# Performance work log

Measured on AMD Instinct MI355X. Metric: run time of the kernel, lower is better.

Reference implementation:

```python
import jax, jax.numpy as jnp
import numpy as np

BS, S, F, H = 512, 128, 136, 128
DISCOUNT = 0.99


def _gru_cell(x, h, Wih, Whh, bih, bhh):
    # torch.nn.GRUCell math; gate order r, z, n
    gi = x @ Wih.T + bih
    gh = h @ Whh.T + bhh
    i_r, i_z, i_n = jnp.split(gi, 3, axis=-1)
    h_r, h_z, h_n = jnp.split(gh, 3, axis=-1)
    r = jax.nn.sigmoid(i_r + h_r)
    z = jax.nn.sigmoid(i_z + h_z)
    n = jnp.tanh(i_n + r * h_n)
    return (1.0 - z) * n + z * h


def _run(batch_ranks, label, fnn_W1, fnn_b1, fnn_W2, fnn_b2,
         cnt_W1, cnt_b1, cnt_W2, cnt_b2, com_W1, com_b1, com_W2, com_b2,
         gru_Wih, gru_Whh, gru_bih, gru_bhh):
    bs, S_, F_ = batch_ranks.shape
    dt = batch_ranks.dtype
    # fnn (Dropout is identity in eval): Linear-ReLU-Linear-Sigmoid
    doc = jax.nn.sigmoid(jax.nn.relu(batch_ranks @ fnn_W1 + fnn_b1) @ fnn_W2 + fnn_b2)  # [bs,S,H]
    H_ = doc.shape[-1]
    pointer = jnp.arange(S_)[None, :]
    h0 = jnp.zeros((bs, H_), dt)
    mask0 = jnp.ones((bs, S_), bool)

    def step(carry, i):
        h, mask = carry
        m3 = mask[:, :, None]
        # stats over still-unselected docs (masked_select equivalent)
        mx = jnp.max(jnp.where(m3, batch_ranks, -jnp.inf), axis=1)            # [bs,F]
        cnt = jnp.sum(mask, axis=1, keepdims=True).astype(dt)
        mn = jnp.sum(jnp.where(m3, batch_ranks, 0.0), axis=1) / cnt           # [bs,F]
        cr = jax.nn.sigmoid(jax.nn.relu(jnp.concatenate([mx, mn], axis=1) @ cnt_W1 + cnt_b1) @ cnt_W2 + cnt_b2)  # [bs,H]
        state = jnp.concatenate([doc,
                                 jnp.broadcast_to(cr[:, None, :], doc.shape),
                                 jnp.broadcast_to(h[:, None, :], doc.shape)], axis=2)  # [bs,S,3H]
        scores = (jax.nn.relu(state @ com_W1 + com_b1) @ com_W2 + com_b2)[..., 0]      # [bs,S]
        p = jax.nn.softmax(scores, axis=-1)        # softmax BEFORE masking, as in source
        p = jnp.where(mask, p, -jnp.inf)
        idx = jnp.argmax(p, axis=-1)               # [bs]
        prob = jnp.max(p, axis=-1)                 # [bs]
        sel = pointer == idx[:, None]              # [bs,S] bool one-hot
        sel_label = jnp.sum(jnp.where(sel, label, 0.0), axis=1)
        reward = (2.0 ** sel_label - 1.0) / jnp.log2(i.astype(dt) + 2.0)
        sel_doc = jnp.einsum('bs,bsh->bh', sel.astype(dt), doc)
        h_new = _gru_cell(sel_doc, h, gru_Wih, gru_Whh, gru_bih, gru_bhh)
        return (h_new, mask & (~sel)), (prob, idx, reward)

    (_, _), (probs, indices, rewards) = jax.lax.scan(step, (h0, mask0), jnp.arange(S_))
    probs = probs.T          # [bs,S]
    indices = indices.T      # [bs,S]
    rewards = rewards.T      # [bs,S]
    rewards = rewards * (DISCOUNT ** jnp.arange(S_, dtype=dt))[None, :]
    R = jnp.flip(jnp.cumsum(jnp.flip(rewards, 1), axis=1), 1)
    loss = -jnp.sum(R * jnp.log(probs))
    sp_loss = -jnp.sum(jax.nn.softmax(label, axis=1) * jax.nn.log_softmax(probs, axis=1))
    ranking = 0.9 ** jnp.argsort(indices, axis=-1).astype(dt)
    return ranking, loss, sp_loss


def setup_inputs() -> dict:
    key = jax.random.key(0)
    ks = jax.random.split(key, 12)
    def lin(k, fi, fo):
        return (jax.random.normal(k, (fi, fo), jnp.float32) / np.sqrt(fi)).astype(jnp.float32)
    return {
        'batch_ranks': jax.random.normal(ks[0], (BS, S, F), jnp.float32),
        'label': jax.random.uniform(ks[1], (BS, S), jnp.float32, 0.0, 4.0),
        'fnn_W1': lin(ks[2], F, H), 'fnn_b1': jnp.zeros((H,), jnp.float32),
        'fnn_W2': lin(ks[3], H, H), 'fnn_b2': jnp.zeros((H,), jnp.float32),
        'cnt_W1': lin(ks[4], 2 * F, H), 'cnt_b1': jnp.zeros((H,), jnp.float32),
        'cnt_W2': lin(ks[5], H, H), 'cnt_b2': jnp.zeros((H,), jnp.float32),
        'com_W1': lin(ks[6], 3 * H, H), 'com_b1': jnp.zeros((H,), jnp.float32),
        'com_W2': lin(ks[7], H, 1), 'com_b2': jnp.zeros((1,), jnp.float32),
        'gru_Wih': (jax.random.normal(ks[8], (3 * H, H), jnp.float32) / np.sqrt(H)),
        'gru_Whh': (jax.random.normal(ks[9], (3 * H, H), jnp.float32) / np.sqrt(H)),
        'gru_bih': jnp.zeros((3 * H,), jnp.float32),
        'gru_bhh': jnp.zeros((3 * H,), jnp.float32),
    }


def reference(batch_ranks, label, fnn_W1, fnn_b1, fnn_W2, fnn_b2,
              cnt_W1, cnt_b1, cnt_W2, cnt_b2, com_W1, com_b1, com_W2, com_b2,
              gru_Wih, gru_Whh, gru_bih, gru_bhh):
    ranking, loss, sp_loss = _run(batch_ranks, label, fnn_W1, fnn_b1, fnn_W2, fnn_b2,
                                  cnt_W1, cnt_b1, cnt_W2, cnt_b2, com_W1, com_b1,
                                  com_W2, com_b2, gru_Wih, gru_Whh, gru_bih, gru_bhh)
    return ranking
```

## Files before the change

kernel.cpp:

```cpp
#include <hip/hip_runtime.h>
#include <math.h>

#define BSZ 512
#define SEQ 128
#define FF  136
#define HH  128

__global__ __launch_bounds__(256) void k_transpose384(const float* __restrict__ A,
                                                      float* __restrict__ At) {
    int i = blockIdx.x * 256 + threadIdx.x;
    if (i < 384 * 128) {
        int r = i >> 7, c = i & 127;
        At[c * 384 + r] = A[i];
    }
}

__global__ __launch_bounds__(256) void k_docvgi(
    const float* __restrict__ br,
    const float* __restrict__ fW1, const float* __restrict__ fb1,
    const float* __restrict__ fW2, const float* __restrict__ fb2,
    const float* __restrict__ comW1,
    const float* __restrict__ WihT, const float* __restrict__ bih,
    float* __restrict__ V, float* __restrict__ GI)
{
    __shared__ float xs[32][FF];
    __shared__ float hs[32][HH];
    __shared__ float ds[32][HH];
    int row0 = blockIdx.x * 32;
    int t = threadIdx.x;
    const float* src = br + (size_t)row0 * FF;
    for (int i = t; i < 32 * FF; i += 256) xs[i / FF][i % FF] = src[i];
    __syncthreads();
    int j = t & 127, rg = t >> 7;
    float acc[16];
#pragma unroll
    for (int r = 0; r < 16; r++) acc[r] = 0.f;
    for (int k = 0; k < FF; k++) {
        float w = fW1[k * HH + j];
#pragma unroll
        for (int r = 0; r < 16; r++) acc[r] += xs[rg + 2 * r][k] * w;
    }
    {
        float bb = fb1[j];
#pragma unroll
        for (int r = 0; r < 16; r++) hs[rg + 2 * r][j] = fmaxf(acc[r] + bb, 0.f);
    }
    __syncthreads();
#pragma unroll
    for (int r = 0; r < 16; r++) acc[r] = 0.f;
    for (int k = 0; k < HH; k++) {
        float w = fW2[k * HH + j];
#pragma unroll
        for (int r = 0; r < 16; r++) acc[r] += hs[rg + 2 * r][k] * w;
    }
    {
        float bb = fb2[j];
#pragma unroll
        for (int r = 0; r < 16; r++)
            ds[rg + 2 * r][j] = 1.f / (1.f + expf(-(acc[r] + bb)));
    }
    __syncthreads();
#pragma unroll
    for (int r = 0; r < 16; r++) acc[r] = 0.f;
    for (int k = 0; k < HH; k++) {
        float w = comW1[k * HH + j];
#pragma unroll
        for (int r = 0; r < 16; r++) acc[r] += ds[rg + 2 * r][k] * w;
    }
#pragma unroll
    for (int r = 0; r < 16; r++) V[(size_t)(row0 + rg + 2 * r) * HH + j] = acc[r];
    for (int p = 0; p < 3; p++) {
        int jj = p * HH + j;
#pragma unroll
        for (int r = 0; r < 16; r++) acc[r] = 0.f;
        for (int k = 0; k < HH; k++) {
            float w = WihT[k * 384 + jj];
#pragma unroll
            for (int r = 0; r < 16; r++) acc[r] += ds[rg + 2 * r][k] * w;
        }
        float bb = bih[jj];
#pragma unroll
        for (int r = 0; r < 16; r++)
            GI[(size_t)(row0 + rg + 2 * r) * 384 + jj] = acc[r] + bb;
    }
}

__global__ __launch_bounds__(256) void k_scan(
    const float* __restrict__ br,
    const float* __restrict__ cntW1, const float* __restrict__ cntb1,
    const float* __restrict__ cntW2, const float* __restrict__ cntb2,
    const float* __restrict__ comW1, const float* __restrict__ comb1,
    const float* __restrict__ comW2,
    const float* __restrict__ WhhT, const float* __restrict__ gbhh,
    const float* __restrict__ V, const float* __restrict__ GI,
    float* __restrict__ out)
{
    __shared__ float  Vl[SEQ][HH + 1];
    __shared__ float  hS[HH], crS[HH], a1S[HH], uS[HH], scS[SEQ], c2S[HH];
    __shared__ float  mxS[FF], mnS[FF];
    __shared__ double smS[FF];
    __shared__ int    mxiS[FF];
    __shared__ int    maskS[SEQ];
    __shared__ float  pp[2][3][HH];
    __shared__ int    selS;

    int b = blockIdx.x;
    int t = threadIdx.x;
    const float* brB = br + (size_t)b * SEQ * FF;
    const float* Vb  = V  + (size_t)b * SEQ * HH;
    const float* GIb = GI + (size_t)b * SEQ * 3 * HH;

    for (int i = t; i < SEQ * HH; i += 256) { int s = i >> 7, j = i & 127; Vl[s][j] = Vb[i]; }
    if (t < HH)  { hS[t] = 0.f; c2S[t] = comW2[t]; }
    if (t < SEQ) maskS[t] = 1;
    if (t < FF) {
        double sm = 0.0; float mx = -__builtin_huge_valf(); int mi = 0;
        for (int s = 0; s < SEQ; s++) {
            float v = brB[s * FF + t];
            sm += (double)v;
            if (v > mx) { mx = v; mi = s; }
        }
        smS[t] = sm; mxS[t] = mx; mxiS[t] = mi;
    }
    __syncthreads();

    int j = t & 127, hf = t >> 7;

    for (int i = 0; i < SEQ; i++) {
        float cntf = (float)(SEQ - i);
        if (t < FF) mnS[t] = ((float)smS[t]) / cntf;
        __syncthreads();

        {
            float acc = 0.f;
            if (hf == 0) {
                for (int k = 0; k < FF; k++) acc += mxS[k] * cntW1[k * HH + j];
            } else {
                for (int k = 0; k < FF; k++) acc += mnS[k] * cntW1[(FF + k) * HH + j];
            }
            pp[hf][0][j] = acc;
        }
        __syncthreads();
        if (t < HH) { float v = pp[0][0][t] + pp[1][0][t] + cntb1[t]; a1S[t] = fmaxf(v, 0.f); }
        __syncthreads();

        {
            float acc = 0.f;
            for (int k = hf * 64; k < hf * 64 + 64; k++) acc += a1S[k] * cntW2[k * HH + j];
            pp[hf][0][j] = acc;
        }
        __syncthreads();
        if (t < HH) { float v = pp[0][0][t] + pp[1][0][t] + cntb2[t]; crS[t] = 1.f / (1.f + expf(-v)); }
        __syncthreads();

        {
            const float* srcv = (hf == 0) ? crS : hS;
            const float* W = comW1 + (size_t)(HH + hf * HH) * HH;
            float acc = 0.f;
            for (int k = 0; k < HH; k++) acc += srcv[k] * W[k * HH + j];
            pp[hf][0][j] = acc;
        }
        __syncthreads();
        if (t < HH) uS[t] = pp[0][0][t] + pp[1][0][t] + comb1[t];
        __syncthreads();

        {
            float acc = 0.f;
            for (int k = hf * 64; k < hf * 64 + 64; k++)
                acc += c2S[k] * fmaxf(Vl[j][k] + uS[k], 0.f);
            pp[hf][0][j] = acc;
        }
        __syncthreads();
        if (t < SEQ) scS[t] = pp[0][0][t] + pp[1][0][t];
        __syncthreads();

        if (t < 64) {
            float v1 = maskS[t]      ? scS[t]      : -__builtin_huge_valf();
            float v2 = maskS[t + 64] ? scS[t + 64] : -__builtin_huge_valf();
            float v; int idx;
            if (v2 > v1) { v = v2; idx = t + 64; } else { v = v1; idx = t; }
            for (int off = 32; off >= 1; off >>= 1) {
                float ov = __shfl_down(v, off);
                int   oi = __shfl_down(idx, off);
                if (ov > v || (ov == v && oi < idx)) { v = ov; idx = oi; }
            }
            if (t == 0) {
                selS = idx;
                maskS[idx] = 0;
                out[(size_t)b * SEQ + idx] = powf(0.9f, (float)i);
            }
        }
        __syncthreads();
        int sel = selS;

        if (t < FF) {
            float rv = brB[sel * FF + t];
            smS[t] -= (double)rv;
            if (sel == mxiS[t] && i < SEQ - 1) {
                float mx = -__builtin_huge_valf(); int mi = 0;
                for (int s = 0; s < SEQ; s++) {
                    if (maskS[s]) { float v = brB[s * FF + t]; if (v > mx) { mx = v; mi = s; } }
                }
                mxS[t] = mx; mxiS[t] = mi;
            }
        }

        {
            float ar = 0.f, az = 0.f, an = 0.f;
            for (int k = hf * 64; k < hf * 64 + 64; k++) {
                float hv = hS[k];
                const float* Wr = WhhT + (size_t)k * 384;
                ar += hv * Wr[j];
                az += hv * Wr[HH + j];
                an += hv * Wr[2 * HH + j];
            }
            pp[hf][0][j] = ar; pp[hf][1][j] = az; pp[hf][2][j] = an;
        }
        __syncthreads();
        if (t < HH) {
            const float* gir = GIb + (size_t)sel * 384;
            float ghr = pp[0][0][t] + pp[1][0][t] + gbhh[t];
            float ghz = pp[0][1][t] + pp[1][1][t] + gbhh[HH + t];
            float ghn = pp[0][2][t] + pp[1][2][t] + gbhh[2 * HH + t];
            float r = 1.f / (1.f + expf(-(gir[t] + ghr)));
            float z = 1.f / (1.f + expf(-(gir[HH + t] + ghz)));
            float n = tanhf(gir[2 * HH + t] + r * ghn);
            float hn = (1.f - z) * n + z * hS[t];
            scS[t] = hn;
        }
        __syncthreads();
        if (t < HH) hS[t] = scS[t];
        __syncthreads();
    }
}

extern "C" void kernel_launch(void* const* d_in, const int* in_sizes, int n_in,
                              void* d_out, int out_size, void* d_ws, size_t ws_size,
                              hipStream_t stream) {
    (void)in_sizes; (void)n_in; (void)out_size; (void)ws_size;
    const float* br    = (const float*)d_in[0];
    const float* fnnW1 = (const float*)d_in[2];
    const float* fnnb1 = (const float*)d_in[3];
    const float* fnnW2 = (const float*)d_in[4];
    const float* fnnb2 = (const float*)d_in[5];
    const float* cntW1 = (const float*)d_in[6];
    const float* cntb1 = (const float*)d_in[7];
    const float* cntW2 = (const float*)d_in[8];
    const float* cntb2 = (const float*)d_in[9];
    const float* comW1 = (const float*)d_in[10];
    const float* comb1 = (const float*)d_in[11];
    const float* comW2 = (const float*)d_in[12];
    const float* Wih   = (const float*)d_in[14];
    const float* Whh   = (const float*)d_in[15];
    const float* bih   = (const float*)d_in[16];
    const float* bhh   = (const float*)d_in[17];

    float* ws   = (float*)d_ws;
    float* V    = ws;
    float* GI   = ws + 8388608;
    float* WihT = ws + 8388608 + 25165824;
    float* WhhT = WihT + 49152;

    hipLaunchKernelGGL(k_transpose384, dim3(192), dim3(256), 0, stream, Wih, WihT);
    hipLaunchKernelGGL(k_transpose384, dim3(192), dim3(256), 0, stream, Whh, WhhT);
    hipLaunchKernelGGL(k_docvgi, dim3(2048), dim3(256), 0, stream,
                       br, fnnW1, fnnb1, fnnW2, fnnb2, comW1, WihT, bih, V, GI);
    hipLaunchKernelGGL(k_scan, dim3(BSZ), dim3(256), 0, stream,
                       br, cntW1, cntb1, cntW2, cntb2, comW1, comb1, comW2,
                       WhhT, bhh, V, GI, (float*)d_out);
}
```

Measured before the change: 3.470 ms.

## Process two batches per block and update cnt first layer incrementally

The scan kernel now handles two batch rows per 1024-thread block, so each weight load serves both rows and more threads share each matvec. The first cnt layer is kept as running double-precision pre-activations for the max and sum parts. Each step subtracts the selected document's contribution and adds corrections only for features whose max changed, instead of recomputing the full 272x128 matvec. This adds more LDS use (two V tiles), atomics for the change list, and many barriers per step, and it may lower occupancy.

```diff
diff --git a/kernel.cpp b/kernel.cpp
--- a/kernel.cpp
+++ b/kernel.cpp
@@ -85,7 +85,7 @@
     }
 }
 
-__global__ __launch_bounds__(256) void k_scan(
+__global__ __launch_bounds__(1024, 4) void k_scan2(
     const float* __restrict__ br,
     const float* __restrict__ cntW1, const float* __restrict__ cntb1,
     const float* __restrict__ cntW2, const float* __restrict__ cntb2,
@@ -95,141 +95,217 @@
     const float* __restrict__ V, const float* __restrict__ GI,
     float* __restrict__ out)
 {
-    __shared__ float  Vl[SEQ][HH + 1];
-    __shared__ float  hS[HH], crS[HH], a1S[HH], uS[HH], scS[SEQ], c2S[HH];
-    __shared__ float  mxS[FF], mnS[FF];
-    __shared__ double smS[FF];
-    __shared__ int    mxiS[FF];
-    __shared__ int    maskS[SEQ];
-    __shared__ float  pp[2][3][HH];
-    __shared__ int    selS;
-
-    int b = blockIdx.x;
-    int t = threadIdx.x;
-    const float* brB = br + (size_t)b * SEQ * FF;
-    const float* Vb  = V  + (size_t)b * SEQ * HH;
-    const float* GIb = GI + (size_t)b * SEQ * 3 * HH;
-
-    for (int i = t; i < SEQ * HH; i += 256) { int s = i >> 7, j = i & 127; Vl[s][j] = Vb[i]; }
-    if (t < HH)  { hS[t] = 0.f; c2S[t] = comW2[t]; }
-    if (t < SEQ) maskS[t] = 1;
-    if (t < FF) {
-        double sm = 0.0; float mx = -__builtin_huge_valf(); int mi = 0;
-        for (int s = 0; s < SEQ; s++) {
-            float v = brB[s * FF + t];
-            sm += (double)v;
-            if (v > mx) { mx = v; mi = s; }
-        }
-        smS[t] = sm; mxS[t] = mx; mxiS[t] = mi;
-    }
-    __syncthreads();
-
-    int j = t & 127, hf = t >> 7;
+    __shared__ double svS[2][HH];
+    __shared__ double mxvS[2][HH];
+    __shared__ float  Vl[2][SEQ][HH + 1];
+    __shared__ float  pp[2][8][HH];
+    __shared__ float  ghp[2][2][384];
+    __shared__ float  hS[2][HH], crS[2][HH], uS[2][HH];
+    __shared__ float  scS[2][SEQ];
+    __shared__ float  mxS[2][FF];
+    __shared__ int    mxiS[2][FF];
+    __shared__ int    maskS[2][SEQ];
+    __shared__ int    chgF[2][FF];
+    __shared__ float  chgD[2][FF];
+    __shared__ int    chgN[2];
+    __shared__ float  pw[SEQ], c2S[HH];
+    __shared__ int    selS[2];
+
+    const int b0 = blockIdx.x * 2;
+    const int t  = threadIdx.x;
+    const float* brB0 = br + (size_t)b0 * SEQ * FF;
+    const float* brB1 = br + (size_t)(b0 + 1) * SEQ * FF;
+
+    for (int g = 0; g < 2; g++) {
+        const float* Vb = V + (size_t)(b0 + g) * SEQ * HH;
+        for (int idx = t; idx < SEQ * HH; idx += 1024)
+            Vl[g][idx >> 7][idx & 127] = Vb[idx];
+    }
+    {
+        int g = t >> 9, r = t & 511;
+        if (r < FF) {
+            const float* bp = (g ? brB1 : brB0) + r;
+            float cs = 0.f; float mx = -__builtin_huge_valf(); int mi = 0;
+            for (int s = 0; s < SEQ; s++) {
+                float v = bp[s * FF];
+                cs += v;
+                if (v > mx) { mx = v; mi = s; }
+            }
+            mxS[g][r] = mx; mxiS[g][r] = mi; chgD[g][r] = cs;
+        }
+    }
+    if (t < SEQ) pw[t] = powf(0.9f, (float)t);
+    if (t < HH)  c2S[t] = comW2[t];
+    if (t < 256) { int g = t >> 7, j = t & 127; hS[g][j] = 0.f; maskS[g][j] = 1; }
+    __syncthreads();
+    if (t < 256) {
+        int g = t >> 7, j = t & 127;
+        double am = 0.0, as = 0.0;
+        for (int f = 0; f < FF; f++) {
+            am += (double)mxS[g][f]  * (double)cntW1[f * HH + j];
+            as += (double)chgD[g][f] * (double)cntW1[(FF + f) * HH + j];
+        }
+        mxvS[g][j] = am; svS[g][j] = as;
+    }
+    __syncthreads();
 
     for (int i = 0; i < SEQ; i++) {
-        float cntf = (float)(SEQ - i);
-        if (t < FF) mnS[t] = ((float)smS[t]) / cntf;
+        if (t < 256) {
+            int g = t >> 7, j = t & 127;
+            if (j == 0) chgN[g] = 0;
+            float pre = (float)(mxvS[g][j] + svS[g][j] / (double)(SEQ - i)) + cntb1[j];
+            scS[g][j] = fmaxf(pre, 0.f);
+        }
         __syncthreads();
 
         {
+            int kg = t >> 7, j = t & 127, k0 = kg * 16;
+            float a0 = 0.f, a1 = 0.f;
+            for (int m = 0; m < 16; m++) {
+                int k = k0 + m;
+                float w = cntW2[k * HH + j];
+                a0 += scS[0][k] * w; a1 += scS[1][k] * w;
+            }
+            pp[0][kg][j] = a0; pp[1][kg][j] = a1;
+        }
+        __syncthreads();
+        if (t < 256) {
+            int g = t >> 7, j = t & 127;
+            float s = pp[g][0][j] + pp[g][1][j] + pp[g][2][j] + pp[g][3][j]
+                    + pp[g][4][j] + pp[g][5][j] + pp[g][6][j] + pp[g][7][j] + cntb2[j];
+            crS[g][j] = 1.f / (1.f + expf(-s));
+        }
+        __syncthreads();
+
+        {
+            int kg = t >> 7, j = t & 127, k0 = kg * 32;
+            const float* base = comW1 + (size_t)(HH + k0) * HH + j;
+            const float* s0p, * s1p;
+            if (kg < 4) { s0p = crS[0] + k0; s1p = crS[1] + k0; }
+            else        { s0p = hS[0] + (k0 - 128); s1p = hS[1] + (k0 - 128); }
+            float a0 = 0.f, a1 = 0.f;
+            for (int m = 0; m < 32; m++) {
+                float w = base[m * HH];
+                a0 += s0p[m] * w; a1 += s1p[m] * w;
+            }
+            pp[0][kg][j] = a0; pp[1][kg][j] = a1;
+        }
+        __syncthreads();
+        if (t < 256) {
+            int g = t >> 7, j = t & 127;
+            uS[g][j] = pp[g][0][j] + pp[g][1][j] + pp[g][2][j] + pp[g][3][j]
+                     + pp[g][4][j] + pp[g][5][j] + pp[g][6][j] + pp[g][7][j] + comb1[j];
+        }
+        __syncthreads();
+
+        {
+            int g = t >> 9, r = t & 511, kg = r >> 7, s = r & 127, k0 = kg * 32;
             float acc = 0.f;
-            if (hf == 0) {
-                for (int k = 0; k < FF; k++) acc += mxS[k] * cntW1[k * HH + j];
-            } else {
-                for (int k = 0; k < FF; k++) acc += mnS[k] * cntW1[(FF + k) * HH + j];
-            }
-            pp[hf][0][j] = acc;
-        }
-        __syncthreads();
-        if (t < HH) { float v = pp[0][0][t] + pp[1][0][t] + cntb1[t]; a1S[t] = fmaxf(v, 0.f); }
+            for (int m = 0; m < 32; m++) {
+                int k = k0 + m;
+                acc += c2S[k] * fmaxf(Vl[g][s][k] + uS[g][k], 0.f);
+            }
+            pp[g][kg][s] = acc;
+        }
+        __syncthreads();
+        if (t < 256) {
+            int g = t >> 7, s = t & 127;
+            scS[g][s] = pp[g][0][s] + pp[g][1][s] + pp[g][2][s] + pp[g][3][s];
+        }
         __syncthreads();
 
         {
-            float acc = 0.f;
-            for (int k = hf * 64; k < hf * 64 + 64; k++) acc += a1S[k] * cntW2[k * HH + j];
-            pp[hf][0][j] = acc;
-        }
-        __syncthreads();
-        if (t < HH) { float v = pp[0][0][t] + pp[1][0][t] + cntb2[t]; crS[t] = 1.f / (1.f + expf(-v)); }
-        __syncthreads();
-
-        {
-            const float* srcv = (hf == 0) ? crS : hS;
-            const float* W = comW1 + (size_t)(HH + hf * HH) * HH;
-            float acc = 0.f;
-            for (int k = 0; k < HH; k++) acc += srcv[k] * W[k * HH + j];
-            pp[hf][0][j] = acc;
-        }
-        __syncthreads();
-        if (t < HH) uS[t] = pp[0][0][t] + pp[1][0][t] + comb1[t];
-        __syncthreads();
-
-        {
-            float acc = 0.f;
-            for (int k = hf * 64; k < hf * 64 + 64; k++)
-                acc += c2S[k] * fmaxf(Vl[j][k] + uS[k], 0.f);
-            pp[hf][0][j] = acc;
-        }
-        __syncthreads();
-        if (t < SEQ) scS[t] = pp[0][0][t] + pp[1][0][t];
-        __syncthreads();
-
-        if (t < 64) {
-            float v1 = maskS[t]      ? scS[t]      : -__builtin_huge_valf();
-            float v2 = maskS[t + 64] ? scS[t + 64] : -__builtin_huge_valf();
-            float v; int idx;
-            if (v2 > v1) { v = v2; idx = t + 64; } else { v = v1; idx = t; }
-            for (int off = 32; off >= 1; off >>= 1) {
-                float ov = __shfl_down(v, off);
-                int   oi = __shfl_down(idx, off);
-                if (ov > v || (ov == v && oi < idx)) { v = ov; idx = oi; }
-            }
-            if (t == 0) {
-                selS = idx;
-                maskS[idx] = 0;
-                out[(size_t)b * SEQ + idx] = powf(0.9f, (float)i);
-            }
-        }
-        __syncthreads();
-        int sel = selS;
-
-        if (t < FF) {
-            float rv = brB[sel * FF + t];
-            smS[t] -= (double)rv;
-            if (sel == mxiS[t] && i < SEQ - 1) {
-                float mx = -__builtin_huge_valf(); int mi = 0;
-                for (int s = 0; s < SEQ; s++) {
-                    if (maskS[s]) { float v = brB[s * FF + t]; if (v > mx) { mx = v; mi = s; } }
-                }
-                mxS[t] = mx; mxiS[t] = mi;
-            }
-        }
-
-        {
-            float ar = 0.f, az = 0.f, an = 0.f;
-            for (int k = hf * 64; k < hf * 64 + 64; k++) {
-                float hv = hS[k];
-                const float* Wr = WhhT + (size_t)k * 384;
-                ar += hv * Wr[j];
-                az += hv * Wr[HH + j];
-                an += hv * Wr[2 * HH + j];
-            }
-            pp[hf][0][j] = ar; pp[hf][1][j] = az; pp[hf][2][j] = an;
-        }
-        __syncthreads();
-        if (t < HH) {
-            const float* gir = GIb + (size_t)sel * 384;
-            float ghr = pp[0][0][t] + pp[1][0][t] + gbhh[t];
-            float ghz = pp[0][1][t] + pp[1][1][t] + gbhh[HH + t];
-            float ghn = pp[0][2][t] + pp[1][2][t] + gbhh[2 * HH + t];
-            float r = 1.f / (1.f + expf(-(gir[t] + ghr)));
-            float z = 1.f / (1.f + expf(-(gir[HH + t] + ghz)));
-            float n = tanhf(gir[2 * HH + t] + r * ghn);
-            float hn = (1.f - z) * n + z * hS[t];
-            scS[t] = hn;
-        }
-        __syncthreads();
-        if (t < HH) hS[t] = scS[t];
+            int gg = -1, lane = 0;
+            if (t < 64)                { gg = 0; lane = t; }
+            else if (t >= 512 && t < 576) { gg = 1; lane = t - 512; }
+            if (gg >= 0) {
+                float v1 = maskS[gg][lane]      ? scS[gg][lane]      : -__builtin_huge_valf();
+                float v2 = maskS[gg][lane + 64] ? scS[gg][lane + 64] : -__builtin_huge_valf();
+                float v; int idx;
+                if (v2 > v1) { v = v2; idx = lane + 64; } else { v = v1; idx = lane; }
+                for (int off = 32; off >= 1; off >>= 1) {
+                    float ov = __shfl_down(v, off);
+                    int   oi = __shfl_down(idx, off);
+                    if (ov > v || (ov == v && oi < idx)) { v = ov; idx = oi; }
+                }
+                if (lane == 0) {
+                    selS[gg] = idx;
+                    maskS[gg][idx] = 0;
+                    out[(size_t)(b0 + gg) * SEQ + idx] = pw[i];
+                }
+            }
+        }
+        __syncthreads();
+
+        if (i < SEQ - 1) {
+            int g = t >> 9, r = t & 511;
+            int sel = selS[g];
+            const float* brB = g ? brB1 : brB0;
+            if (r < FF) {
+                int f = r;
+                if (sel == mxiS[g][f]) {
+                    float om = mxS[g][f];
+                    float mx = -__builtin_huge_valf(); int mi = 0;
+                    for (int s = 0; s < SEQ; s++) {
+                        if (maskS[g][s]) {
+                            float v = brB[s * FF + f];
+                            if (v > mx) { mx = v; mi = s; }
+                        }
+                    }
+                    mxS[g][f] = mx; mxiS[g][f] = mi;
+                    int e = atomicAdd(&chgN[g], 1);
+                    chgF[g][e] = f; chgD[g][e] = mx - om;
+                }
+            } else if (r >= 256) {
+                int kg = (r >> 7) - 2, j = r & 127;
+                const float* brow = brB + (size_t)sel * FF;
+                float acc = 0.f;
+                int k0 = kg * 68;
+                for (int m = 0; m < 68; m++) {
+                    int k = k0 + m;
+                    acc += brow[k] * cntW1[(FF + k) * HH + j];
+                }
+                pp[g][4 + kg][j] = acc;
+            }
+        }
+        __syncthreads();
+
+        if (i < SEQ - 1 && t < 256) {
+            int g = t >> 7, j = t & 127;
+            svS[g][j] -= (double)(pp[g][4][j] + pp[g][5][j]);
+            int n = chgN[g];
+            double acc = mxvS[g][j];
+            for (int e = 0; e < n; e++)
+                acc += (double)chgD[g][e] * (double)cntW1[chgF[g][e] * HH + j];
+            mxvS[g][j] = acc;
+        }
+        __syncthreads();
+
+        if (i < SEQ - 1) {
+            if (t < 768) {
+                int kg = t / 384, jj = t % 384, k0 = kg * 64;
+                const float* Wp = WhhT + (size_t)k0 * 384 + jj;
+                float a0 = 0.f, a1 = 0.f;
+                for (int m = 0; m < 64; m++) {
+                    float w = Wp[m * 384];
+                    a0 += hS[0][k0 + m] * w; a1 += hS[1][k0 + m] * w;
+                }
+                ghp[0][kg][jj] = a0; ghp[1][kg][jj] = a1;
+            }
+        }
+        __syncthreads();
+        if (i < SEQ - 1 && t < 256) {
+            int g = t >> 7, j = t & 127;
+            int sel = selS[g];
+            const float* gir = GI + ((size_t)(b0 + g) * SEQ + sel) * 384;
+            float ghr = ghp[g][0][j]       + ghp[g][1][j]       + gbhh[j];
+            float ghz = ghp[g][0][HH + j]  + ghp[g][1][HH + j]  + gbhh[HH + j];
+            float ghn = ghp[g][0][2*HH + j]+ ghp[g][1][2*HH + j]+ gbhh[2*HH + j];
+            float rr = 1.f / (1.f + expf(-(gir[j] + ghr)));
+            float zz = 1.f / (1.f + expf(-(gir[HH + j] + ghz)));
+            float nn = tanhf(gir[2 * HH + j] + rr * ghn);
+            hS[g][j] = (1.f - zz) * nn + zz * hS[g][j];
+        }
         __syncthreads();
     }
 }
@@ -265,7 +341,7 @@
     hipLaunchKernelGGL(k_transpose384, dim3(192), dim3(256), 0, stream, Whh, WhhT);
     hipLaunchKernelGGL(k_docvgi, dim3(2048), dim3(256), 0, stream,
                        br, fnnW1, fnnb1, fnnW2, fnnb2, comW1, WihT, bih, V, GI);
-    hipLaunchKernelGGL(k_scan, dim3(BSZ), dim3(256), 0, stream,
+    hipLaunchKernelGGL(k_scan2, dim3(BSZ / 2), dim3(1024), 0, stream,
                        br, cntW1, cntb1, cntW2, cntb2, comW1, comb1, comW2,
                        WhhT, bhh, V, GI, (float*)d_out);
 }
```

Result: slower. 7.341 ms (+111.6%).

## Incrementally update count-layer preactivation and overlap GRU matvec with scan stages

Applied to the files above, without the earlier changes.

The first count-network layer is no longer recomputed from full max and mean vectors every step. The kernel keeps running double-precision partial sums: the mean term is updated by subtracting the selected row's projection, and the max term is updated only for features whose maximum changed, tracked with an atomic change list. The block grows to 512 threads so the GRU hidden matvec runs alongside the count-layer matvec, and the GRU update runs alongside the max recompute. This cuts per-step FLOPs and barrier count, at the cost of more shared memory, fewer resident blocks, and possible numerical drift from incremental accumulation.

```diff
diff --git a/kernel.cpp b/kernel.cpp
--- a/kernel.cpp
+++ b/kernel.cpp
@@ -85,7 +85,7 @@
     }
 }
 
-__global__ __launch_bounds__(256) void k_scan(
+__global__ __launch_bounds__(512, 4) void k_scan3(
     const float* __restrict__ br,
     const float* __restrict__ cntW1, const float* __restrict__ cntb1,
     const float* __restrict__ cntW2, const float* __restrict__ cntb2,
@@ -96,87 +96,112 @@
     float* __restrict__ out)
 {
     __shared__ float  Vl[SEQ][HH + 1];
-    __shared__ float  hS[HH], crS[HH], a1S[HH], uS[HH], scS[SEQ], c2S[HH];
-    __shared__ float  mxS[FF], mnS[FF];
-    __shared__ double smS[FF];
-    __shared__ int    mxiS[FF];
-    __shared__ int    maskS[SEQ];
-    __shared__ float  pp[2][3][HH];
-    __shared__ int    selS;
-
-    int b = blockIdx.x;
-    int t = threadIdx.x;
+    __shared__ double svS[HH], mxvS[HH];
+    __shared__ float  a1S[HH], crS[HH], uS[HH], hS[HH], c2S[HH];
+    __shared__ float  ghS[256];
+    __shared__ float  ghp2[2][HH];
+    __shared__ float  ppB[2][HH], ppC[4][HH], ppD[4][HH];
+    __shared__ float  svp[HH];
+    __shared__ float  mxS[FF], chgD[FF];
+    __shared__ int    mxiS[FF], chgF[FF], maskS[SEQ];
+    __shared__ int    selS, chgN;
+
+    const int b = blockIdx.x;
+    const int t = threadIdx.x;
     const float* brB = br + (size_t)b * SEQ * FF;
-    const float* Vb  = V  + (size_t)b * SEQ * HH;
-    const float* GIb = GI + (size_t)b * SEQ * 3 * HH;
-
-    for (int i = t; i < SEQ * HH; i += 256) { int s = i >> 7, j = i & 127; Vl[s][j] = Vb[i]; }
+    const float* GIb = GI + (size_t)b * SEQ * 384;
+
+    {
+        const float* Vb = V + (size_t)b * SEQ * HH;
+        for (int idx = t; idx < SEQ * HH; idx += 512)
+            Vl[idx >> 7][idx & 127] = Vb[idx];
+    }
     if (t < HH)  { hS[t] = 0.f; c2S[t] = comW2[t]; }
     if (t < SEQ) maskS[t] = 1;
     if (t < FF) {
-        double sm = 0.0; float mx = -__builtin_huge_valf(); int mi = 0;
+        float cs = 0.f; float mx = -__builtin_huge_valf(); int mi = 0;
+        const float* bp = brB + t;
         for (int s = 0; s < SEQ; s++) {
-            float v = brB[s * FF + t];
-            sm += (double)v;
+            float v = bp[s * FF];
+            cs += v;
             if (v > mx) { mx = v; mi = s; }
         }
-        smS[t] = sm; mxS[t] = mx; mxiS[t] = mi;
-    }
-    __syncthreads();
-
-    int j = t & 127, hf = t >> 7;
+        mxS[t] = mx; mxiS[t] = mi; chgD[t] = cs;
+    }
+    if (t == 256) chgN = 0;
+    __syncthreads();
+    if (t < HH) {
+        double am = 0.0, as = 0.0;
+        for (int f = 0; f < FF; f++) {
+            am += (double)mxS[f]  * (double)cntW1[f * HH + t];
+            as += (double)chgD[f] * (double)cntW1[(FF + f) * HH + t];
+        }
+        mxvS[t] = am; svS[t] = as;
+        a1S[t] = fmaxf((float)(am + as / 128.0) + cntb1[t], 0.f);
+    }
+    __syncthreads();
 
     for (int i = 0; i < SEQ; i++) {
-        float cntf = (float)(SEQ - i);
-        if (t < FF) mnS[t] = ((float)smS[t]) / cntf;
+        if (t < 256) {
+            int kh = t >> 7, j = t & 127;
+            const float* W = cntW2 + (size_t)(kh * 64) * HH + j;
+            const float* a = a1S + kh * 64;
+            float acc = 0.f;
+            for (int m = 0; m < 64; m++) acc += a[m] * W[m * HH];
+            ppB[kh][j] = acc;
+        } else {
+            int jj = t - 256;
+            const float* W = WhhT + jj;
+            float acc = 0.f;
+            for (int k = 0; k < 128; k++) acc += hS[k] * W[k * 384];
+            ghS[jj] = acc;
+        }
+        __syncthreads();
+
+        if (t < HH) {
+            crS[t] = 1.f / (1.f + expf(-(ppB[0][t] + ppB[1][t] + cntb2[t])));
+        } else if (t == HH) {
+            chgN = 0;
+        } else if (t >= 256) {
+            int r = t - 256, kh = r >> 7, j = r & 127;
+            const float* W = WhhT + 256 + j;
+            const float* h = hS + kh * 64;
+            float acc = 0.f;
+            for (int m = 0; m < 64; m++) acc += h[m] * W[(kh * 64 + m) * 384];
+            ghp2[kh][j] = acc;
+        }
         __syncthreads();
 
         {
-            float acc = 0.f;
-            if (hf == 0) {
-                for (int k = 0; k < FF; k++) acc += mxS[k] * cntW1[k * HH + j];
-            } else {
-                for (int k = 0; k < FF; k++) acc += mnS[k] * cntW1[(FF + k) * HH + j];
+            int q = t >> 7, j = t & 127;
+            const float* W = comW1 + (size_t)(HH + q * 64) * HH + j;
+            const float* s0 = (q < 2) ? (crS + q * 64) : (hS + (q - 2) * 64);
+            float acc = 0.f;
+            for (int m = 0; m < 64; m++) acc += s0[m] * W[m * HH];
+            ppC[q][j] = acc;
+        }
+        __syncthreads();
+
+        if (t < HH) uS[t] = ppC[0][t] + ppC[1][t] + ppC[2][t] + ppC[3][t] + comb1[t];
+        __syncthreads();
+
+        {
+            int q = t >> 7, s = t & 127, k0 = q * 32;
+            float acc = 0.f;
+            for (int m = 0; m < 32; m++) {
+                int k = k0 + m;
+                acc += c2S[k] * fmaxf(Vl[s][k] + uS[k], 0.f);
             }
-            pp[hf][0][j] = acc;
-        }
-        __syncthreads();
-        if (t < HH) { float v = pp[0][0][t] + pp[1][0][t] + cntb1[t]; a1S[t] = fmaxf(v, 0.f); }
-        __syncthreads();
-
-        {
-            float acc = 0.f;
-            for (int k = hf * 64; k < hf * 64 + 64; k++) acc += a1S[k] * cntW2[k * HH + j];
-            pp[hf][0][j] = acc;
-        }
-        __syncthreads();
-        if (t < HH) { float v = pp[0][0][t] + pp[1][0][t] + cntb2[t]; crS[t] = 1.f / (1.f + expf(-v)); }
-        __syncthreads();
-
-        {
-            const float* srcv = (hf == 0) ? crS : hS;
-            const float* W = comW1 + (size_t)(HH + hf * HH) * HH;
-            float acc = 0.f;
-            for (int k = 0; k < HH; k++) acc += srcv[k] * W[k * HH + j];
-            pp[hf][0][j] = acc;
-        }
-        __syncthreads();
-        if (t < HH) uS[t] = pp[0][0][t] + pp[1][0][t] + comb1[t];
-        __syncthreads();
-
-        {
-            float acc = 0.f;
-            for (int k = hf * 64; k < hf * 64 + 64; k++)
-                acc += c2S[k] * fmaxf(Vl[j][k] + uS[k], 0.f);
-            pp[hf][0][j] = acc;
-        }
-        __syncthreads();
-        if (t < SEQ) scS[t] = pp[0][0][t] + pp[1][0][t];
+            ppD[q][s] = acc;
+        }
+        __syncthreads();
+
+        if (t < SEQ) ppD[0][t] = ppD[0][t] + ppD[1][t] + ppD[2][t] + ppD[3][t];
         __syncthreads();
 
         if (t < 64) {
-            float v1 = maskS[t]      ? scS[t]      : -__builtin_huge_valf();
-            float v2 = maskS[t + 64] ? scS[t + 64] : -__builtin_huge_valf();
+            float v1 = maskS[t]      ? ppD[0][t]      : -__builtin_huge_valf();
+            float v2 = maskS[t + 64] ? ppD[0][t + 64] : -__builtin_huge_valf();
             float v; int idx;
             if (v2 > v1) { v = v2; idx = t + 64; } else { v = v1; idx = t; }
             for (int off = 32; off >= 1; off >>= 1) {
@@ -193,43 +218,50 @@
         __syncthreads();
         int sel = selS;
 
-        if (t < FF) {
-            float rv = brB[sel * FF + t];
-            smS[t] -= (double)rv;
-            if (sel == mxiS[t] && i < SEQ - 1) {
-                float mx = -__builtin_huge_valf(); int mi = 0;
-                for (int s = 0; s < SEQ; s++) {
-                    if (maskS[s]) { float v = brB[s * FF + t]; if (v > mx) { mx = v; mi = s; } }
+        if (i < SEQ - 1) {
+            if (t < FF) {
+                if (sel == mxiS[t]) {
+                    float om = mxS[t];
+                    float mx = -__builtin_huge_valf(); int mi = 0;
+                    const float* bp = brB + t;
+                    for (int s = 0; s < SEQ; s++) {
+                        if (maskS[s]) { float v = bp[s * FF]; if (v > mx) { mx = v; mi = s; } }
+                    }
+                    mxS[t] = mx; mxiS[t] = mi;
+                    int e = atomicAdd(&chgN, 1);
+                    chgF[e] = t; chgD[e] = mx - om;
                 }
-                mxS[t] = mx; mxiS[t] = mi;
+            } else if (t >= 256 && t < 384) {
+                int j = t - 256;
+                const float* brow = brB + (size_t)sel * FF;
+                const float* W = cntW1 + (size_t)FF * HH + j;
+                float acc = 0.f;
+                for (int k = 0; k < FF; k++) acc += brow[k] * W[k * HH];
+                svp[j] = acc;
+            } else if (t >= 384) {
+                int j = t - 384;
+                const float* gir = GIb + (size_t)sel * 384;
+                float ghr = ghS[j]           + gbhh[j];
+                float ghz = ghS[HH + j]      + gbhh[HH + j];
+                float ghn = ghp2[0][j] + ghp2[1][j] + gbhh[2 * HH + j];
+                float rr = 1.f / (1.f + expf(-(gir[j] + ghr)));
+                float zz = 1.f / (1.f + expf(-(gir[HH + j] + ghz)));
+                float nn = tanhf(gir[2 * HH + j] + rr * ghn);
+                hS[j] = (1.f - zz) * nn + zz * hS[j];
             }
         }
-
-        {
-            float ar = 0.f, az = 0.f, an = 0.f;
-            for (int k = hf * 64; k < hf * 64 + 64; k++) {
-                float hv = hS[k];
-                const float* Wr = WhhT + (size_t)k * 384;
-                ar += hv * Wr[j];
-                az += hv * Wr[HH + j];
-                an += hv * Wr[2 * HH + j];
-            }
-            pp[hf][0][j] = ar; pp[hf][1][j] = az; pp[hf][2][j] = an;
-        }
-        __syncthreads();
-        if (t < HH) {
-            const float* gir = GIb + (size_t)sel * 384;
-            float ghr = pp[0][0][t] + pp[1][0][t] + gbhh[t];
-            float ghz = pp[0][1][t] + pp[1][1][t] + gbhh[HH + t];
-            float ghn = pp[0][2][t] + pp[1][2][t] + gbhh[2 * HH + t];
-            float r = 1.f / (1.f + expf(-(gir[t] + ghr)));
-            float z = 1.f / (1.f + expf(-(gir[HH + t] + ghz)));
-            float n = tanhf(gir[2 * HH + t] + r * ghn);
-            float hn = (1.f - z) * n + z * hS[t];
-            scS[t] = hn;
-        }
-        __syncthreads();
-        if (t < HH) hS[t] = scS[t];
+        __syncthreads();
+
+        if (i < SEQ - 1 && t < HH) {
+            double acc = mxvS[t];
+            int n = chgN;
+            for (int e = 0; e < n; e++)
+                acc += (double)chgD[e] * (double)cntW1[chgF[e] * HH + t];
+            mxvS[t] = acc;
+            double sv = svS[t] - (double)svp[t];
+            svS[t] = sv;
+            a1S[t] = fmaxf((float)(acc + sv / (double)(SEQ - 1 - i)) + cntb1[t], 0.f);
+        }
         __syncthreads();
     }
 }
@@ -265,7 +297,7 @@
     hipLaunchKernelGGL(k_transpose384, dim3(192), dim3(256), 0, stream, Whh, WhhT);
     hipLaunchKernelGGL(k_docvgi, dim3(2048), dim3(256), 0, stream,
                        br, fnnW1, fnnb1, fnnW2, fnnb2, comW1, WihT, bih, V, GI);
-    hipLaunchKernelGGL(k_scan, dim3(BSZ), dim3(256), 0, stream,
+    hipLaunchKernelGGL(k_scan3, dim3(BSZ), dim3(512), 0, stream,
                        br, cntW1, cntb1, cntW2, cntb2, comW1, comb1, comW2,
                        WhhT, bhh, V, GI, (float*)d_out);
 }
```

After: 13.53 ms. 290% more time.
